# Optimization experiments

Hardware: AMD Instinct MI355X
Metric: run time of the kernel (lower is better)

## Reference

```python
import jax, jax.numpy as jnp
import numpy as np

# Model constants (match init_kwargs)
NUM_HEADS = 8
IN_BITS = 64
N_STATE = 256
N_OUT = 64
K_CONN = 8            # n_bits_per_output_neuron
HASH = 65536          # hash_size
K_BITS = 3            # routing key bits
B = 128               # batch of independent sequences
T = 128               # timesteps (windows) per sequence


def setup_inputs() -> dict:
    key = jax.random.key(0)
    k1, k2, k3, k4, k5, k6 = jax.random.split(key, 6)
    # flat bit sequences, split into T windows of IN_BITS in reference()
    bits = jax.random.randint(k1, (B, T * IN_BITS), 0, 2, dtype=jnp.int32)
    # state layer: full connectivity (default n_bits_per_state_neuron =
    # input_bits + n_state_neurons), hashed addressing via random odd-ish
    # integer coefficients dotted with the bit vector, mod HASH.
    total_in = IN_BITS + N_STATE  # 320
    state_coeffs = jax.random.randint(k2, (N_STATE, total_in), 1, HASH, dtype=jnp.int32)
    state_mem = jax.random.uniform(k3, (N_STATE, HASH), dtype=jnp.float32)
    # output heads: each neuron connects to K_CONN random state bits
    head_conn = jax.random.randint(k4, (NUM_HEADS, N_OUT, K_CONN), 0, N_STATE, dtype=jnp.int32)
    head_coeffs = jax.random.randint(k5, (NUM_HEADS, N_OUT, K_CONN), 1, HASH, dtype=jnp.int32)
    head_mem = jax.random.uniform(k6, (NUM_HEADS, N_OUT, HASH), dtype=jnp.float32)
    return {
        "bits": bits,
        "state_coeffs": state_coeffs,
        "state_mem": state_mem,
        "head_conn": head_conn,
        "head_coeffs": head_coeffs,
        "head_mem": head_mem,
    }


def reference(bits, state_coeffs, state_mem, head_conn, head_coeffs, head_mem):
    # windows: [B, T, IN_BITS]
    windows = bits.reshape(B, T, IN_BITS)
    n_state, hash_size = state_mem.shape

    def step(state, w):  # state: [B, N_STATE] int32 bits; w: [B, IN_BITS]
        x = jnp.concatenate([w, state], axis=1)                 # [B, IN+N]
        addr = (x @ state_coeffs.T) % hash_size                 # hashed address [B, N]
        vals = state_mem[jnp.arange(n_state), addr]             # gather [B, N]
        new_state = (vals >= 0.5).astype(jnp.int32)             # RAM output bits
        return new_state, None

    state0 = jnp.zeros((B, n_state), jnp.int32)
    final_state, _ = jax.lax.scan(step, state0, jnp.swapaxes(windows, 0, 1))

    # all output heads read the shared final state
    sel = final_state[:, head_conn]                             # [B, H, O, K]
    addr_h = jnp.einsum('bhok,hok->bho', sel, head_coeffs) % hash_size
    head_vals = head_mem[jnp.arange(NUM_HEADS)[:, None],
                         jnp.arange(N_OUT)[None, :], addr_h]    # [B, H, O]

    # kv routing: pack last K_BITS bits of the final window (MSB first)
    last_w = windows[:, -1, :]
    pow2 = 2 ** jnp.arange(K_BITS - 1, -1, -1)
    head_idx = jnp.sum(last_w[:, -K_BITS:] * pow2, axis=1) % NUM_HEADS  # [B]

    out = head_vals[jnp.arange(B), head_idx]                    # [B, N_OUT]
    return out
```

## Files before the change

### kernel.cpp

```cpp
#include <hip/hip_runtime.h>
#include <stdint.h>

#define T_ 128

typedef int v4i __attribute__((ext_vector_type(4)));

__global__ void prep_bfrag(const int* __restrict__ sc, uint4* __restrict__ bf) {
  int gid = blockIdx.x * 256 + threadIdx.x;
  if (gid >= 160 * 64) return;
  int mf = gid >> 6, l = gid & 63;
  int tau = mf / 10, rem = mf % 10;
  int kap = rem >> 1, h = rem & 1;
  int j = 16 * tau + (l & 15);
  int kinb = (l >> 4) * 16;
  unsigned wout[4];
#pragma unroll
  for (int r = 0; r < 4; ++r) {
    unsigned wrd = 0;
#pragma unroll
    for (int be = 0; be < 4; ++be) {
      int kin = kinb + 4 * r + be;
      int col = (kap == 0) ? kin : 64 + ((kap - 1) << 6) + kin;
      unsigned c = (unsigned)sc[j * 320 + col];
      unsigned byte = (h ? (c >> 8) : c) & 0xFFu;
      byte = (byte - 128u) & 0xFFu;
      wrd |= byte << (8 * be);
    }
    wout[r] = wrd;
  }
  bf[gid] = make_uint4(wout[0], wout[1], wout[2], wout[3]);
}

__global__ void prep_wbits(const int* __restrict__ bits,
                           unsigned long long* __restrict__ wb) {
  int gid = blockIdx.x * 256 + threadIdx.x;
  int wv = gid >> 6, lane = gid & 63;
  unsigned long long m = __ballot(bits[gid] != 0);
  if (lane == 0) wb[wv] = m;
}

__global__ void prep_bitpack(const float* __restrict__ sm,
                             unsigned long long* __restrict__ packed) {
  int base = blockIdx.x * (256 * 32) + threadIdx.x;
  int lane = threadIdx.x & 63;
#pragma unroll 1
  for (int it = 0; it < 32; ++it) {
    int idx = base + it * 256;
    float v = sm[idx];
    unsigned long long m = __ballot(v >= 0.5f);
    if (lane == 0) packed[idx >> 6] = m;
  }
}

static __device__ __forceinline__ v4i expand16(unsigned b16) {
  v4i a;
#pragma unroll
  for (int r = 0; r < 4; ++r) {
    unsigned nib = (b16 >> (4 * r)) & 0xFu;
    a[r] = (int)((nib * 0x00204081u) & 0x01010101u);
  }
  return a;
}

__global__ __launch_bounds__(512, 2) void scan_heads(
    const uint4* __restrict__ bfrag,
    const unsigned long long* __restrict__ wbits,
    const unsigned* __restrict__ packed32,
    const int* __restrict__ head_conn,
    const int* __restrict__ head_coeffs,
    const float* __restrict__ head_mem,
    float* __restrict__ out) {
  __shared__ __align__(16) unsigned msh[2][8];
  const int tid = threadIdx.x;
  const int b = blockIdx.x;
  const int w = tid >> 6, l = tid & 63;
  const int qq = (l >> 4) & 3;
  const int sh = 16 * (qq & 1);
  const int wi = qq >> 1;

  v4i bf[2][5][2];
#pragma unroll
  for (int i = 0; i < 2; ++i)
#pragma unroll
    for (int k = 0; k < 5; ++k)
#pragma unroll
      for (int h = 0; h < 2; ++h) {
        int mf = ((2 * w + i) * 5 + k) * 2 + h;
        bf[i][k][h] = __builtin_bit_cast(v4i, bfrag[mf * 64 + l]);
      }

  unsigned words[8];
#pragma unroll
  for (int i = 0; i < 8; ++i) words[i] = 0u;
  unsigned long long wcur = wbits[b * 128];

  v4i acc[2][2];
  {
    v4i aw = expand16((unsigned)((wcur >> (16 * qq)) & 0xFFFFu));
    v4i z = (v4i){0, 0, 0, 0};
#pragma unroll
    for (int i = 0; i < 2; ++i)
#pragma unroll
      for (int h = 0; h < 2; ++h)
        acc[i][h] = __builtin_amdgcn_mfma_i32_16x16x64_i8(aw, bf[i][0][h], z, 0, 0, 0);
  }

#pragma unroll 1
  for (int t = 0; t < T_; ++t) {
    unsigned NB = (unsigned)__popcll(wcur);
#pragma unroll
    for (int i = 0; i < 8; ++i) {
      unsigned sw = (unsigned)__builtin_amdgcn_readfirstlane((int)words[i]);
      NB += (unsigned)__popc((int)sw);
    }

#pragma unroll
    for (int c = 0; c < 4; ++c) {
      v4i a = expand16((words[2 * c + wi] >> sh) & 0xFFFFu);
      acc[0][0] = __builtin_amdgcn_mfma_i32_16x16x64_i8(a, bf[0][c + 1][0], acc[0][0], 0, 0, 0);
      acc[0][1] = __builtin_amdgcn_mfma_i32_16x16x64_i8(a, bf[0][c + 1][1], acc[0][1], 0, 0, 0);
      acc[1][0] = __builtin_amdgcn_mfma_i32_16x16x64_i8(a, bf[1][c + 1][0], acc[1][0], 0, 0, 0);
      acc[1][1] = __builtin_amdgcn_mfma_i32_16x16x64_i8(a, bf[1][c + 1][1], acc[1][1], 0, 0, 0);
    }

    int tn = (t + 1 < T_) ? t + 1 : t;
    unsigned long long wnext = wbits[b * 128 + tn];

    unsigned corr = (NB * 32896u) & 0xFFFFu;
    unsigned lo = (unsigned)((l & 16) ? acc[1][0][0] : acc[0][0][0]);
    unsigned hi = (unsigned)((l & 16) ? acc[1][1][0] : acc[0][1][0]);
    unsigned ad = (lo + (hi << 8) + corr) & 0xFFFFu;

    unsigned bitv = 0;
    if (l < 32) {
      unsigned word = packed32[((size_t)(32 * w + l) << 11) + (ad >> 5)];
      bitv = (word >> (ad & 31)) & 1u;
    }
    unsigned long long mq = __ballot(bitv != 0u);
    if (l == 0) msh[t & 1][w] = (unsigned)mq;

    {
      v4i aw = expand16((unsigned)((wnext >> (16 * qq)) & 0xFFFFu));
      v4i z = (v4i){0, 0, 0, 0};
#pragma unroll
      for (int i = 0; i < 2; ++i)
#pragma unroll
        for (int h = 0; h < 2; ++h)
          acc[i][h] = __builtin_amdgcn_mfma_i32_16x16x64_i8(aw, bf[i][0][h], z, 0, 0, 0);
    }

    __syncthreads();

    uint4 u0 = *((const uint4*)&msh[t & 1][0]);
    uint4 u1 = *((const uint4*)&msh[t & 1][4]);
    words[0] = u0.x; words[1] = u0.y; words[2] = u0.z; words[3] = u0.w;
    words[4] = u1.x; words[5] = u1.y; words[6] = u1.z; words[7] = u1.w;
    wcur = wnext;
  }

  if (w == 0) {
    int h = (int)((((wcur >> 61) & 1) << 2) | (((wcur >> 62) & 1) << 1) |
                  ((wcur >> 63) & 1));
    int ho = h * 64 + l;
    const int4* cn4 = (const int4*)(head_conn + ho * 8);
    const int4* cf4 = (const int4*)(head_coeffs + ho * 8);
    int4 cna = cn4[0], cnb = cn4[1];
    int4 cfa = cf4[0], cfb = cf4[1];
    int cns[8] = {cna.x, cna.y, cna.z, cna.w, cnb.x, cnb.y, cnb.z, cnb.w};
    int cfs[8] = {cfa.x, cfa.y, cfa.z, cfa.w, cfb.x, cfb.y, cfb.z, cfb.w};
    unsigned addr = 0;
#pragma unroll
    for (int k = 0; k < 8; ++k) {
      unsigned bit = (words[cns[k] >> 5] >> (cns[k] & 31)) & 1u;
      addr += bit * (unsigned)cfs[k];
    }
    addr &= 0xFFFFu;
    out[b * 64 + l] = head_mem[((size_t)ho << 16) + addr];
  }
}

extern "C" void kernel_launch(void* const* d_in, const int* in_sizes, int n_in,
                              void* d_out, int out_size, void* d_ws, size_t ws_size,
                              hipStream_t stream) {
  const int*   bits         = (const int*)d_in[0];
  const int*   state_coeffs = (const int*)d_in[1];
  const float* state_mem    = (const float*)d_in[2];
  const int*   head_conn    = (const int*)d_in[3];
  const int*   head_coeffs  = (const int*)d_in[4];
  const float* head_mem     = (const float*)d_in[5];
  float* out = (float*)d_out;

  char* ws = (char*)d_ws;
  uint4*              bfrag  = (uint4*)ws;
  unsigned long long* wbits  = (unsigned long long*)(ws + (160 << 10));
  unsigned*           packed = (unsigned*)(ws + (288 << 10));

  prep_bfrag<<<40, 256, 0, stream>>>(state_coeffs, bfrag);
  prep_wbits<<<4096, 256, 0, stream>>>(bits, wbits);
  prep_bitpack<<<2048, 256, 0, stream>>>(state_mem, (unsigned long long*)packed);
  scan_heads<<<128, 512, 0, stream>>>(bfrag, wbits, packed,
                                      head_conn, head_coeffs, head_mem, out);
}
```

Before: 352.1 us.

## Split state neurons across 16 waves with one 16-neuron tile each

Doubles the block from 8 to 16 waves so each wave owns one 16-neuron tile instead of two. That halves the per-wave MFMA chain and register footprint per timestep. Each wave now publishes a 16-bit mask into shared memory, and the state words are reassembled from 16-bit pieces. The trade-off is a per-step __syncthreads across twice as many waves, and more waves per block competing for the CU.

```diff
diff --git a/kernel.cpp b/kernel.cpp
--- a/kernel.cpp
+++ b/kernel.cpp
@@ -62,7 +62,7 @@
   return a;
 }
 
-__global__ __launch_bounds__(512, 2) void scan_heads(
+__global__ __launch_bounds__(1024, 4) void scan_heads(
     const uint4* __restrict__ bfrag,
     const unsigned long long* __restrict__ wbits,
     const unsigned* __restrict__ packed32,
@@ -70,7 +70,7 @@
     const int* __restrict__ head_coeffs,
     const float* __restrict__ head_mem,
     float* __restrict__ out) {
-  __shared__ __align__(16) unsigned msh[2][8];
+  __shared__ __align__(16) unsigned short msh16[2][16];
   const int tid = threadIdx.x;
   const int b = blockIdx.x;
   const int w = tid >> 6, l = tid & 63;
@@ -78,31 +78,28 @@
   const int sh = 16 * (qq & 1);
   const int wi = qq >> 1;
 
-  v4i bf[2][5][2];
+  v4i bf[5][2];
 #pragma unroll
-  for (int i = 0; i < 2; ++i)
+  for (int k = 0; k < 5; ++k)
 #pragma unroll
-    for (int k = 0; k < 5; ++k)
-#pragma unroll
-      for (int h = 0; h < 2; ++h) {
-        int mf = ((2 * w + i) * 5 + k) * 2 + h;
-        bf[i][k][h] = __builtin_bit_cast(v4i, bfrag[mf * 64 + l]);
-      }
+    for (int h = 0; h < 2; ++h) {
+      int mf = (w * 5 + k) * 2 + h;
+      bf[k][h] = __builtin_bit_cast(v4i, bfrag[mf * 64 + l]);
+    }
+
+  const size_t rowbase = ((size_t)(16 * w + (l & 15)) << 11);
 
   unsigned words[8];
 #pragma unroll
   for (int i = 0; i < 8; ++i) words[i] = 0u;
   unsigned long long wcur = wbits[b * 128];
 
-  v4i acc[2][2];
+  v4i acc0, acc1;
   {
     v4i aw = expand16((unsigned)((wcur >> (16 * qq)) & 0xFFFFu));
     v4i z = (v4i){0, 0, 0, 0};
-#pragma unroll
-    for (int i = 0; i < 2; ++i)
-#pragma unroll
-      for (int h = 0; h < 2; ++h)
-        acc[i][h] = __builtin_amdgcn_mfma_i32_16x16x64_i8(aw, bf[i][0][h], z, 0, 0, 0);
+    acc0 = __builtin_amdgcn_mfma_i32_16x16x64_i8(aw, bf[0][0], z, 0, 0, 0);
+    acc1 = __builtin_amdgcn_mfma_i32_16x16x64_i8(aw, bf[0][1], z, 0, 0, 0);
   }
 
 #pragma unroll 1
@@ -117,42 +114,35 @@
 #pragma unroll
     for (int c = 0; c < 4; ++c) {
       v4i a = expand16((words[2 * c + wi] >> sh) & 0xFFFFu);
-      acc[0][0] = __builtin_amdgcn_mfma_i32_16x16x64_i8(a, bf[0][c + 1][0], acc[0][0], 0, 0, 0);
-      acc[0][1] = __builtin_amdgcn_mfma_i32_16x16x64_i8(a, bf[0][c + 1][1], acc[0][1], 0, 0, 0);
-      acc[1][0] = __builtin_amdgcn_mfma_i32_16x16x64_i8(a, bf[1][c + 1][0], acc[1][0], 0, 0, 0);
-      acc[1][1] = __builtin_amdgcn_mfma_i32_16x16x64_i8(a, bf[1][c + 1][1], acc[1][1], 0, 0, 0);
+      acc0 = __builtin_amdgcn_mfma_i32_16x16x64_i8(a, bf[c + 1][0], acc0, 0, 0, 0);
+      acc1 = __builtin_amdgcn_mfma_i32_16x16x64_i8(a, bf[c + 1][1], acc1, 0, 0, 0);
     }
 
     int tn = (t + 1 < T_) ? t + 1 : t;
     unsigned long long wnext = wbits[b * 128 + tn];
 
     unsigned corr = (NB * 32896u) & 0xFFFFu;
-    unsigned lo = (unsigned)((l & 16) ? acc[1][0][0] : acc[0][0][0]);
-    unsigned hi = (unsigned)((l & 16) ? acc[1][1][0] : acc[0][1][0]);
-    unsigned ad = (lo + (hi << 8) + corr) & 0xFFFFu;
+    unsigned ad = ((unsigned)acc0[0] + ((unsigned)acc1[0] << 8) + corr) & 0xFFFFu;
 
     unsigned bitv = 0;
-    if (l < 32) {
-      unsigned word = packed32[((size_t)(32 * w + l) << 11) + (ad >> 5)];
+    if (l < 16) {
+      unsigned word = packed32[rowbase + (ad >> 5)];
       bitv = (word >> (ad & 31)) & 1u;
     }
     unsigned long long mq = __ballot(bitv != 0u);
-    if (l == 0) msh[t & 1][w] = (unsigned)mq;
+    if (l == 0) msh16[t & 1][w] = (unsigned short)(mq & 0xFFFFu);
 
     {
       v4i aw = expand16((unsigned)((wnext >> (16 * qq)) & 0xFFFFu));
       v4i z = (v4i){0, 0, 0, 0};
-#pragma unroll
-      for (int i = 0; i < 2; ++i)
-#pragma unroll
-        for (int h = 0; h < 2; ++h)
-          acc[i][h] = __builtin_amdgcn_mfma_i32_16x16x64_i8(aw, bf[i][0][h], z, 0, 0, 0);
+      acc0 = __builtin_amdgcn_mfma_i32_16x16x64_i8(aw, bf[0][0], z, 0, 0, 0);
+      acc1 = __builtin_amdgcn_mfma_i32_16x16x64_i8(aw, bf[0][1], z, 0, 0, 0);
     }
 
     __syncthreads();
 
-    uint4 u0 = *((const uint4*)&msh[t & 1][0]);
-    uint4 u1 = *((const uint4*)&msh[t & 1][4]);
+    uint4 u0 = ((const uint4*)&msh16[t & 1][0])[0];
+    uint4 u1 = ((const uint4*)&msh16[t & 1][0])[1];
     words[0] = u0.x; words[1] = u0.y; words[2] = u0.z; words[3] = u0.w;
     words[4] = u1.x; words[5] = u1.y; words[6] = u1.z; words[7] = u1.w;
     wcur = wnext;
@@ -198,6 +188,6 @@
   prep_bfrag<<<40, 256, 0, stream>>>(state_coeffs, bfrag);
   prep_wbits<<<4096, 256, 0, stream>>>(bits, wbits);
   prep_bitpack<<<2048, 256, 0, stream>>>(state_mem, (unsigned long long*)packed);
-  scan_heads<<<128, 512, 0, stream>>>(bfrag, wbits, packed,
-                                      head_conn, head_coeffs, head_mem, out);
+  scan_heads<<<128, 1024, 0, stream>>>(bfrag, wbits, packed,
+                                       head_conn, head_coeffs, head_mem, out);
 }
```

Result: slower. 397.2 us (+12.8%).
